# Performance work log

Measured on AMD Instinct MI355X. Metric: run time of the kernel, lower is better.

## Reference

```python
import jax, jax.numpy as jnp
import numpy as np

B, T, D = 32, 512, 768
K, H = 256, 512


def setup_inputs() -> dict:
    key = jax.random.key(0)
    ks = jax.random.split(key, 5)
    s = 0.02  # keep pre-activations in a sane range
    return {
        "inputs": jax.random.normal(ks[0], (B, T, D), jnp.float32),
        "W_x": jax.random.normal(ks[1], (K + 1, 4 * H), jnp.float32) * s,
        "W_h": jax.random.normal(ks[2], (H, 4 * H), jnp.float32) * s,
        "b_lstm": jnp.zeros((4 * H,), jnp.float32),
        "W_key": jax.random.normal(ks[3], (H, K), jnp.float32) * s,
        "b_key": jnp.zeros((K,), jnp.float32),
        "W_g": jax.random.normal(ks[4], (H, 1), jnp.float32) * s,
        "b_g": jnp.zeros((1,), jnp.float32),
        "conf_gain": jnp.ones((), jnp.float32),
        "conf_bias": jnp.zeros((), jnp.float32),
    }


def reference(inputs, W_x, W_h, b_lstm, W_key, b_key, W_g, b_g, conf_gain, conf_bias):
    Bq, Tq, Dq = inputs.shape
    Kq = W_key.shape[1]
    Hq = W_h.shape[0]
    t_idx = jnp.arange(Tq)
    xs = jnp.transpose(inputs, (1, 0, 2))  # [T, B, D]

    def step(carry, xt):
        t, x = xt  # t: scalar step index, x: [B, D]
        key_r, h, c, M_k, M_v = carry
        # Keras LSTMCell (gate order i, f, c, o); input is previous key_r [B, K+1]
        z = key_r @ W_x + h @ W_h + b_lstm
        i, f, g_c, o = jnp.split(z, 4, axis=-1)
        i = jax.nn.sigmoid(i)
        f = jax.nn.sigmoid(f)
        g_c = jnp.tanh(g_c)
        o = jax.nn.sigmoid(o)
        c = f * c + i * g_c
        h = o * jnp.tanh(c)  # lstm_out == hidden in Keras LSTMCell
        key_w = h @ W_key + b_key            # [B, K]
        g = jax.nn.sigmoid(h @ W_g + b_g)    # [B, 1]
        # similarity attention over all previously written memory slots
        sim = jnp.einsum('bd,tbd->bt', x, M_v)          # [B, T]
        mask = (t_idx < t)[None, :]                     # valid slots only
        w_k = jax.nn.softmax(jnp.where(mask, sim, -1e30), axis=1)
        c_k = jax.nn.sigmoid(sim * conf_gain + conf_bias)
        aug = jnp.concatenate([jnp.transpose(M_k, (1, 0, 2)), c_k[:, :, None]], axis=2)  # [B, T, K+1]
        key_r_new = jnp.where(t > 0, g * jnp.einsum('bt,btk->bk', w_k, aug), 0.0)
        M_k = M_k.at[t].set(key_w)
        M_v = M_v.at[t].set(x)
        return (key_r_new, h, c, M_k, M_v), None

    init = (
        jnp.zeros((Bq, Kq + 1), inputs.dtype),
        jnp.zeros((Bq, Hq), inputs.dtype),
        jnp.zeros((Bq, Hq), inputs.dtype),
        jnp.zeros((Tq, Bq, Kq), inputs.dtype),
        jnp.zeros((Tq, Bq, Dq), inputs.dtype),
    )
    (key_r, h, c, M_k, M_v), _ = jax.lax.scan(step, init, (t_idx, xs))
    return h  # final lstm_out
```

## Files before the change

kernel.cpp:

```cpp
#include <hip/hip_runtime.h>
#include <math.h>

#define BQ 32
#define TQ 512
#define DQ 768
#define KQ 256
#define HQ 512
#define G4 2048
#define SROW 772
#define NWG 512
#define NTHR 256
#define NBG 4

typedef float f32x4 __attribute__((ext_vector_type(4)));

__device__ __forceinline__ void waitcnt0() {
  asm volatile("s_waitcnt vmcnt(0) lgkmcnt(0)" ::: "memory");
}
__device__ __forceinline__ void st_agent(float* p, float v) {
  asm volatile("global_store_dword %0, %1, off sc0 sc1" :: "v"(p), "v"(v) : "memory");
}
__device__ __forceinline__ int ld_flag(const int* p) {
  int v;
  asm volatile("global_load_dword %0, %1, off sc0 sc1\ns_waitcnt vmcnt(0)"
               : "=v"(v) : "v"(p) : "memory");
  return v;
}
__device__ __forceinline__ void wg_wait(const int* flags, int target) {
  const int lane = threadIdx.x & 63;
  for (;;) {
    int v = ld_flag(flags + lane);
    if (__all(v >= target)) break;
    __builtin_amdgcn_s_sleep(1);
  }
  __syncthreads();
}
__device__ __forceinline__ void wg_signal(int* flag, int val) {
  waitcnt0();
  __syncthreads();
  if (threadIdx.x == 0)
    asm volatile("global_store_dword %0, %1, off sc0 sc1" :: "v"(flag), "v"(val) : "memory");
}
__device__ __forceinline__ float sigm(float x) { return 1.f / (1.f + __expf(-x)); }

__global__ void __launch_bounds__(256) gram_k(const float* __restrict__ X,
                                              float* __restrict__ Gm) {
  __shared__ __align__(16) float As[64 * 33];
  __shared__ __align__(16) float Bs[64 * 33];
  const int bid = blockIdx.x;
  const int b = blockIdx.y;
  int I = 0, base = 0;
  while (base + I + 1 <= bid) { base += I + 1; ++I; }
  const int J = bid - base;
  const int t0 = I * 64, u0 = J * 64;
  const float* Xb = X + (size_t)b * TQ * DQ;
  const int ty = threadIdx.x >> 4, tx = threadIdx.x & 15;
  const int sc = threadIdx.x & 31, sr = threadIdx.x >> 5;
  float acc[4][4];
#pragma unroll
  for (int i = 0; i < 4; ++i)
#pragma unroll
    for (int j = 0; j < 4; ++j) acc[i][j] = 0.f;
  for (int k0 = 0; k0 < DQ; k0 += 32) {
#pragma unroll
    for (int rr = 0; rr < 8; ++rr) {
      const int r = rr * 8 + sr;
      As[r * 33 + sc] = Xb[(size_t)(t0 + r) * DQ + k0 + sc];
      Bs[r * 33 + sc] = Xb[(size_t)(u0 + r) * DQ + k0 + sc];
    }
    __syncthreads();
#pragma unroll
    for (int k = 0; k < 32; ++k) {
      float av[4], bv[4];
#pragma unroll
      for (int i = 0; i < 4; ++i) av[i] = As[(ty * 4 + i) * 33 + k];
#pragma unroll
      for (int j = 0; j < 4; ++j) bv[j] = Bs[(tx * 4 + j) * 33 + k];
#pragma unroll
      for (int i = 0; i < 4; ++i)
#pragma unroll
        for (int j = 0; j < 4; ++j) acc[i][j] += av[i] * bv[j];
    }
    __syncthreads();
  }
  float* gb = Gm + (size_t)b * TQ * TQ;
#pragma unroll
  for (int i = 0; i < 4; ++i) {
    f32x4 o;
    o.x = acc[i][0]; o.y = acc[i][1]; o.z = acc[i][2]; o.w = acc[i][3];
    *(f32x4*)&gb[(size_t)(t0 + ty * 4 + i) * TQ + u0 + tx * 4] = o;
  }
}

__global__ void __launch_bounds__(256) smax_k(float* __restrict__ Gm,
                                              float* __restrict__ Sv,
                                              const float* __restrict__ cgp,
                                              const float* __restrict__ cbp) {
  const int t = blockIdx.x + 1;
  const int b = blockIdx.y;
  const int tid = threadIdx.x;
  const int lane = tid & 63;
  const int wv = tid >> 6;
  __shared__ float row[TQ];
  __shared__ float r1[4], r2[4], r3[4];
  float* R = Gm + ((size_t)b * TQ + t) * TQ;
  const float cg = cgp[0], cb = cbp[0];
  for (int i = tid; i < t; i += 256) row[i] = R[i];
  __syncthreads();
  float m = -3e38f;
  for (int i = tid; i < t; i += 256) m = fmaxf(m, row[i]);
#pragma unroll
  for (int k = 1; k < 64; k <<= 1) m = fmaxf(m, __shfl_xor(m, k));
  if (lane == 0) r1[wv] = m;
  __syncthreads();
  m = fmaxf(fmaxf(r1[0], r1[1]), fmaxf(r1[2], r1[3]));
  float s = 0.f, sck = 0.f;
  for (int i = tid; i < t; i += 256) {
    const float r = row[i];
    const float e = __expf(r - m);
    const float ck = 1.f / (1.f + __expf(-(r * cg + cb)));
    row[i] = e; s += e; sck += e * ck;
  }
#pragma unroll
  for (int k = 1; k < 64; k <<= 1) { s += __shfl_xor(s, k); sck += __shfl_xor(sck, k); }
  if (lane == 0) { r2[wv] = s; r3[wv] = sck; }
  __syncthreads();
  s = r2[0] + r2[1] + r2[2] + r2[3];
  sck = r3[0] + r3[1] + r3[2] + r3[3];
  const float inv = 1.f / s;
  for (int i = tid; i < t; i += 256) R[i] = row[i] * inv;
  if (tid == 0) Sv[(size_t)b * TQ + t] = sck * inv;
}

__global__ void __launch_bounds__(NTHR, 2) esbn_scan(
    const float* __restrict__ Wx, const float* __restrict__ Wh,
    const float* __restrict__ bl, const float* __restrict__ Wk,
    const float* __restrict__ bk, const float* __restrict__ Wg,
    const float* __restrict__ bgp, const float* __restrict__ Wmat,
    const float* __restrict__ Sv, float* buf, int* flagsX, int* flagsY,
    float* __restrict__ out) {
  __shared__ __align__(16) float st[NBG * SROW];
  __shared__ __align__(16) float wrow[NBG * TQ];
  __shared__ __align__(16) float Mk_s[16 * 520];
  __shared__ __align__(16) float wkey_s[4 * 520];
  __shared__ float wgv[HQ];
  __shared__ __align__(16) float zred[4 * 8 * 4 * 4];
  __shared__ float c_s[NBG * 8];
  __shared__ float gg_s[NBG];
  __shared__ float A_s[NBG * 4];
  __shared__ float bl_s[32];
  __shared__ float bk_s[4];
  __shared__ float bg_s;

  const int tid = threadIdx.x;
  const int wg = blockIdx.x & 63;
  const int grp = blockIdx.x >> 6;
  const int b0 = grp * NBG;
  const int dc = tid >> 3;
  const int cg = tid & 7;

  int colg[4];
#pragma unroll
  for (int j = 0; j < 4; ++j) {
    const int c = cg * 4 + j;
    colg[j] = (c >> 3) * HQ + wg * 8 + (c & 7);
  }
  f32x4 wh[16], wxr[8], wxl;
#pragma unroll
  for (int i = 0; i < 16; ++i) {
    const int d = (i << 5) + dc;
    wh[i].x = Wh[(size_t)d * G4 + colg[0]];
    wh[i].y = Wh[(size_t)d * G4 + colg[1]];
    wh[i].z = Wh[(size_t)d * G4 + colg[2]];
    wh[i].w = Wh[(size_t)d * G4 + colg[3]];
  }
#pragma unroll
  for (int i = 0; i < 8; ++i) {
    const int d = (i << 5) + dc;
    wxr[i].x = Wx[(size_t)d * G4 + colg[0]];
    wxr[i].y = Wx[(size_t)d * G4 + colg[1]];
    wxr[i].z = Wx[(size_t)d * G4 + colg[2]];
    wxr[i].w = Wx[(size_t)d * G4 + colg[3]];
  }
  wxl.x = wxl.y = wxl.z = wxl.w = 0.f;
  if (dc == 0) {
    wxl.x = Wx[(size_t)256 * G4 + colg[0]];
    wxl.y = Wx[(size_t)256 * G4 + colg[1]];
    wxl.z = Wx[(size_t)256 * G4 + colg[2]];
    wxl.w = Wx[(size_t)256 * G4 + colg[3]];
  }
  for (int i = tid; i < NBG * SROW; i += NTHR) st[i] = 0.f;
  for (int i = tid; i < 16 * 520; i += NTHR) Mk_s[i] = 0.f;
  for (int i = tid; i < 4 * 520; i += NTHR) {
    const int kl = i / 520, u = i - kl * 520;
    wkey_s[i] = (u < HQ) ? Wk[(size_t)u * KQ + wg * 4 + kl] : 0.f;
  }
  for (int i = tid; i < HQ; i += NTHR) wgv[i] = Wg[i];
  if (tid < 32) bl_s[tid] = bl[(tid >> 3) * HQ + wg * 8 + (tid & 7)];
  if (tid < 4) bk_s[tid] = bk[wg * 4 + tid];
  if (tid == 0) bg_s = bgp[0];
  if (tid < NBG * 8) c_s[tid] = 0.f;
  if (tid < NBG * 4) A_s[tid] = 0.f;
  __syncthreads();

  int* fx = flagsX + grp * 64;
  int* fy = flagsY + grp * 64;
  const int yb = tid >> 6;
  const int ykl = (tid >> 4) & 3;
  const int ytc = tid & 15;
  const int lt = tid & 63;

  for (int t = 0; t < TQ; ++t) {
    const int p = t & 1, pn = p ^ 1;
    f32x4 acc[NBG];
#pragma unroll
    for (int b = 0; b < NBG; ++b) { acc[b].x = 0.f; acc[b].y = 0.f; acc[b].z = 0.f; acc[b].w = 0.f; }
#pragma unroll
    for (int i = 0; i < 16; ++i) {
      const f32x4 w = wh[i];
      const int d = (i << 5) + dc;
#pragma unroll
      for (int b = 0; b < NBG; ++b) acc[b] += st[b * SROW + d] * w;
    }
    wg_wait(fy, t);
    {
      float* base = buf + (size_t)(p * BQ + b0) * SROW;
      const int r0 = tid / 65, o0 = tid - r0 * 65;
      const float* q0 = base + r0 * SROW + 512 + (o0 << 2);
      f32x4 u0, u1;
      u1.x = u1.y = u1.z = u1.w = 0.f;
      asm volatile("global_load_dwordx4 %0, %1, off sc0 sc1" : "=v"(u0) : "v"(q0));
      if (tid < 4) {
        const int j1 = tid + 256;
        const int r1 = j1 / 65, o1 = j1 - r1 * 65;
        const float* q1 = base + r1 * SROW + 512 + (o1 << 2);
        asm volatile("global_load_dwordx4 %0, %1, off sc0 sc1" : "=v"(u1) : "v"(q1));
      }
      asm volatile("s_waitcnt vmcnt(0)" : "+v"(u0), "+v"(u1) : : "memory");
      *(f32x4*)&st[r0 * SROW + 512 + (o0 << 2)] = u0;
      if (tid < 4) {
        const int j1 = tid + 256;
        const int r1 = j1 / 65, o1 = j1 - r1 * 65;
        *(f32x4*)&st[r1 * SROW + 512 + (o1 << 2)] = u1;
      }
    }
    __syncthreads();
#pragma unroll
    for (int i = 0; i < 8; ++i) {
      const f32x4 w = wxr[i];
      const int d = 512 + (i << 5) + dc;
#pragma unroll
      for (int b = 0; b < NBG; ++b) acc[b] += st[b * SROW + d] * w;
    }
    if (dc == 0) {
#pragma unroll
      for (int b = 0; b < NBG; ++b) acc[b] += st[b * SROW + 768] * wxl;
    }
#pragma unroll
    for (int m = 8; m <= 32; m <<= 1) {
#pragma unroll
      for (int b = 0; b < NBG; ++b) {
        acc[b].x += __shfl_xor(acc[b].x, m);
        acc[b].y += __shfl_xor(acc[b].y, m);
        acc[b].z += __shfl_xor(acc[b].z, m);
        acc[b].w += __shfl_xor(acc[b].w, m);
      }
    }
    if (lt < 8) {
      const int wv = tid >> 6;
#pragma unroll
      for (int b = 0; b < NBG; ++b)
        *(f32x4*)&zred[((wv * 8 + lt) * 4 + b) * 4] = acc[b];
    }
    __syncthreads();
    if (tid < 32) {
      const int b = tid >> 3, u = tid & 7;
      float zg[4];
#pragma unroll
      for (int g = 0; g < 4; ++g) {
        const int cgi = g * 2 + (u >> 2), comp = u & 3;
        float z = bl_s[g * 8 + u];
#pragma unroll
        for (int wv = 0; wv < 4; ++wv) z += zred[((wv * 8 + cgi) * 4 + b) * 4 + comp];
        zg[g] = z;
      }
      const float gi = sigm(zg[0]);
      const float gf = sigm(zg[1]);
      const float go = sigm(zg[3]);
      const float cn = gf * c_s[tid] + gi * tanhf(zg[2]);
      const float hv = go * tanhf(cn);
      c_s[tid] = cn;
      st_agent(buf + (size_t)(pn * BQ + b0 + b) * SROW + wg * 8 + u, hv);
      if (t == TQ - 1) out[(size_t)(b0 + b) * HQ + wg * 8 + u] = hv;
    }
    wg_signal(&fx[wg], t + 1);
    if (t == TQ - 1) break;

    if (t > 0) {
      const float* wr = Wmat + ((size_t)(b0 + yb) * TQ + t) * TQ;
#pragma unroll
      for (int k = 0; k < 8; ++k) {
        const int u = lt + (k << 6);
        wrow[yb * TQ + u] = (u < t) ? wr[u] : 0.f;
      }
    }
    __syncthreads();
    float accA = 0.f;
    if (t > 0) {
      const float* mk = &Mk_s[(yb * 4 + ykl) * 520];
      const float* wb = &wrow[yb * TQ];
#pragma unroll
      for (int j = 0; j < 32; ++j) {
        const int u = ytc + (j << 4);
        accA += wb[u] * mk[u];
      }
      accA += __shfl_xor(accA, 1);
      accA += __shfl_xor(accA, 2);
      accA += __shfl_xor(accA, 4);
      accA += __shfl_xor(accA, 8);
    }
    if (ytc == 0) A_s[yb * 4 + ykl] = accA;
    wg_wait(fx, t + 1);
    {
      float* base = buf + (size_t)(pn * BQ + b0) * SROW;
      f32x4 v0, v1;
      const int i0 = tid, i1 = tid + 256;
      const float* p0 = base + (i0 >> 7) * SROW + ((i0 & 127) << 2);
      const float* p1v = base + (i1 >> 7) * SROW + ((i1 & 127) << 2);
      asm volatile("global_load_dwordx4 %0, %1, off sc0 sc1" : "=v"(v0) : "v"(p0));
      asm volatile("global_load_dwordx4 %0, %1, off sc0 sc1" : "=v"(v1) : "v"(p1v));
      asm volatile("s_waitcnt vmcnt(0)" : "+v"(v0), "+v"(v1) : : "memory");
      *(f32x4*)&st[(i0 >> 7) * SROW + ((i0 & 127) << 2)] = v0;
      *(f32x4*)&st[(i1 >> 7) * SROW + ((i1 & 127) << 2)] = v1;
    }
    __syncthreads();
    {
      float a = 0.f;
#pragma unroll
      for (int k = 0; k < 8; ++k) {
        const int u = lt + (k << 6);
        a += st[yb * SROW + u] * wgv[u];
      }
#pragma unroll
      for (int m = 1; m <= 32; m <<= 1) a += __shfl_xor(a, m);
      if (lt == 0) gg_s[yb] = sigm(a + bg_s);
    }
    __syncthreads();
    if (ytc == 0)
      st_agent(buf + (size_t)(pn * BQ + b0 + yb) * SROW + 512 + wg * 4 + ykl,
               gg_s[yb] * A_s[yb * 4 + ykl]);
    if (wg == 63 && lt == 0)
      st_agent(buf + (size_t)(pn * BQ + b0 + yb) * SROW + 512 + 256,
               gg_s[yb] * Sv[(size_t)(b0 + yb) * TQ + t]);
    wg_signal(&fy[wg], t + 1);
    {
      float kw = 0.f;
      const float* hrow = &st[yb * SROW];
      const float* wkr = &wkey_s[ykl * 520];
#pragma unroll
      for (int j = 0; j < 32; ++j) {
        const int u = ytc + (j << 4);
        kw += hrow[u] * wkr[u];
      }
      kw += __shfl_xor(kw, 1);
      kw += __shfl_xor(kw, 2);
      kw += __shfl_xor(kw, 4);
      kw += __shfl_xor(kw, 8);
      if (ytc == 0) Mk_s[(yb * 4 + ykl) * 520 + t] = kw + bk_s[ykl];
    }
  }
}

extern "C" void kernel_launch(void* const* d_in, const int* in_sizes, int n_in,
                              void* d_out, int out_size, void* d_ws, size_t ws_size,
                              hipStream_t stream) {
  (void)in_sizes; (void)n_in; (void)out_size; (void)ws_size;
  const float* X  = (const float*)d_in[0];
  const float* Wx = (const float*)d_in[1];
  const float* Wh = (const float*)d_in[2];
  const float* bl = (const float*)d_in[3];
  const float* Wk = (const float*)d_in[4];
  const float* bk = (const float*)d_in[5];
  const float* Wg = (const float*)d_in[6];
  const float* bg = (const float*)d_in[7];
  const float* cg = (const float*)d_in[8];
  const float* cb = (const float*)d_in[9];
  float* out = (float*)d_out;
  float* ws = (float*)d_ws;

  float* Gm = ws;
  float* Sv = ws + (size_t)8388608;
  float* buf = ws + (size_t)8404992;
  int* flagsX = (int*)(ws + (size_t)8454400);
  int* flagsY = flagsX + 512;

  hipMemsetAsync(Sv, 0, (size_t)(16384 + 49408 + 1024) * 4, stream);
  gram_k<<<dim3(36, BQ), dim3(256), 0, stream>>>(X, Gm);
  smax_k<<<dim3(TQ - 1, BQ), dim3(256), 0, stream>>>(Gm, Sv, cg, cb);

  void* args[] = {(void*)&Wx, (void*)&Wh, (void*)&bl, (void*)&Wk, (void*)&bk,
                  (void*)&Wg, (void*)&bg, (void*)&Gm, (void*)&Sv,
                  (void*)&buf, (void*)&flagsX, (void*)&flagsY, (void*)&out};
  hipError_t e = hipLaunchCooperativeKernel((const void*)esbn_scan, dim3(NWG),
                                            dim3(NTHR), args, 0, stream);
  if (e != hipSuccess) {
    esbn_scan<<<dim3(NWG), dim3(NTHR), 0, stream>>>(Wx, Wh, bl, Wk, bk, Wg, bg,
                                                    Gm, Sv, buf, flagsX,
                                                    flagsY, out);
  }
}
```

Before: 4.876 ms.

## Fold W_key into W_x and cut scan to one grid barrier per step

Precomputes Wc = W_key·W_x[:K] and bk·W_x so that key_r·W_x is rewritten as g·(attention-weighted h history)·Wc plus bias and confidence terms. Each workgroup stores its own h history slice in shared memory as int16 and computes the weighted history sum locally. This removes the second cross-workgroup flag wait and the per-step key projection. It also remaps blocks so a group's workgroups interleave. The risks are precision loss from 16-bit quantized h and an extra GEMM setup kernel.

```diff
diff --git a/kernel.cpp b/kernel.cpp
--- a/kernel.cpp
+++ b/kernel.cpp
@@ -7,10 +7,10 @@
 #define KQ 256
 #define HQ 512
 #define G4 2048
-#define SROW 772
 #define NWG 512
 #define NTHR 256
 #define NBG 4
+#define PROW 1028
 
 typedef float f32x4 __attribute__((ext_vector_type(4)));
 
@@ -24,6 +24,11 @@
   int v;
   asm volatile("global_load_dword %0, %1, off sc0 sc1\ns_waitcnt vmcnt(0)"
                : "=v"(v) : "v"(p) : "memory");
+  return v;
+}
+__device__ __forceinline__ f32x4 ldx4(const float* p) {
+  f32x4 v;
+  asm volatile("global_load_dwordx4 %0, %1, off sc0 sc1" : "=v"(v) : "v"(p) : "memory");
   return v;
 }
 __device__ __forceinline__ void wg_wait(const int* flags, int target) {
@@ -34,12 +39,6 @@
     __builtin_amdgcn_s_sleep(1);
   }
   __syncthreads();
-}
-__device__ __forceinline__ void wg_signal(int* flag, int val) {
-  waitcnt0();
-  __syncthreads();
-  if (threadIdx.x == 0)
-    asm volatile("global_store_dword %0, %1, off sc0 sc1" :: "v"(flag), "v"(val) : "memory");
 }
 __device__ __forceinline__ float sigm(float x) { return 1.f / (1.f + __expf(-x)); }
 
@@ -132,29 +131,79 @@
   if (tid == 0) Sv[(size_t)b * TQ + t] = sck * inv;
 }
 
+__global__ void __launch_bounds__(256) wcomb_k(const float* __restrict__ Wkey,
+                                               const float* __restrict__ Wx,
+                                               float* __restrict__ Wc) {
+  __shared__ __align__(16) float As[64 * 33];
+  __shared__ __align__(16) float Bs[64 * 33];
+  const int c0 = blockIdx.x * 64, u0 = blockIdx.y * 64;
+  const int ty = threadIdx.x >> 4, tx = threadIdx.x & 15;
+  const int sc = threadIdx.x & 31, sr = threadIdx.x >> 5;
+  float acc[4][4];
+#pragma unroll
+  for (int i = 0; i < 4; ++i)
+#pragma unroll
+    for (int j = 0; j < 4; ++j) acc[i][j] = 0.f;
+  for (int k0 = 0; k0 < KQ; k0 += 32) {
+#pragma unroll
+    for (int rr = 0; rr < 8; ++rr) {
+      const int r = rr * 8 + sr;
+      As[r * 33 + sc] = Wkey[(size_t)(u0 + r) * KQ + k0 + sc];
+      Bs[r * 33 + sc] = Wx[(size_t)(k0 + sc) * G4 + c0 + r];
+    }
+    __syncthreads();
+#pragma unroll
+    for (int k = 0; k < 32; ++k) {
+      float av[4], bv[4];
+#pragma unroll
+      for (int i = 0; i < 4; ++i) av[i] = As[(ty * 4 + i) * 33 + k];
+#pragma unroll
+      for (int j = 0; j < 4; ++j) bv[j] = Bs[(tx * 4 + j) * 33 + k];
+#pragma unroll
+      for (int i = 0; i < 4; ++i)
+#pragma unroll
+        for (int j = 0; j < 4; ++j) acc[i][j] += av[i] * bv[j];
+    }
+    __syncthreads();
+  }
+#pragma unroll
+  for (int i = 0; i < 4; ++i) {
+    f32x4 o;
+    o.x = acc[i][0]; o.y = acc[i][1]; o.z = acc[i][2]; o.w = acc[i][3];
+    *(f32x4*)&Wc[(size_t)(u0 + ty * 4 + i) * G4 + c0 + tx * 4] = o;
+  }
+}
+
+__global__ void __launch_bounds__(256) bkwx_k(const float* __restrict__ bk,
+                                              const float* __restrict__ Wx,
+                                              float* __restrict__ bw) {
+  const int col = blockIdx.x * 256 + threadIdx.x;
+  float a = 0.f;
+  for (int k = 0; k < KQ; ++k) a += bk[k] * Wx[(size_t)k * G4 + col];
+  bw[col] = a;
+}
+
 __global__ void __launch_bounds__(NTHR, 2) esbn_scan(
     const float* __restrict__ Wx, const float* __restrict__ Wh,
     const float* __restrict__ bl, const float* __restrict__ Wk,
     const float* __restrict__ bk, const float* __restrict__ Wg,
     const float* __restrict__ bgp, const float* __restrict__ Wmat,
-    const float* __restrict__ Sv, float* buf, int* flagsX, int* flagsY,
+    const float* __restrict__ Sv, const float* __restrict__ Wc,
+    const float* __restrict__ bw, float* buf, int* flags,
     float* __restrict__ out) {
-  __shared__ __align__(16) float st[NBG * SROW];
-  __shared__ __align__(16) float wrow[NBG * TQ];
-  __shared__ __align__(16) float Mk_s[16 * 520];
-  __shared__ __align__(16) float wkey_s[4 * 520];
+  __shared__ short hh[32 * 520];
+  __shared__ __align__(16) float st_h[NBG * 512];
+  __shared__ __align__(16) float st_q[NBG * 512];
+  __shared__ __align__(16) float wrow[NBG * 512];
   __shared__ float wgv[HQ];
-  __shared__ __align__(16) float zred[4 * 8 * 4 * 4];
-  __shared__ float c_s[NBG * 8];
-  __shared__ float gg_s[NBG];
-  __shared__ float A_s[NBG * 4];
-  __shared__ float bl_s[32];
-  __shared__ float bk_s[4];
+  __shared__ __align__(16) float zred[4 * 8 * 4 * 8];
+  __shared__ float bl_s[32], e_s[32], l_s[32], c_s[32];
+  __shared__ float gg_s[NBG], sv_s[NBG];
   __shared__ float bg_s;
 
   const int tid = threadIdx.x;
-  const int wg = blockIdx.x & 63;
-  const int grp = blockIdx.x >> 6;
+  const int grp = blockIdx.x & 7;
+  const int wg = blockIdx.x >> 3;
   const int b0 = grp * NBG;
   const int dc = tid >> 3;
   const int cg = tid & 7;
@@ -165,7 +214,7 @@
     const int c = cg * 4 + j;
     colg[j] = (c >> 3) * HQ + wg * 8 + (c & 7);
   }
-  f32x4 wh[16], wxr[8], wxl;
+  f32x4 wh[16], wc[16];
 #pragma unroll
   for (int i = 0; i < 16; ++i) {
     const int d = (i << 5) + dc;
@@ -174,199 +223,202 @@
     wh[i].z = Wh[(size_t)d * G4 + colg[2]];
     wh[i].w = Wh[(size_t)d * G4 + colg[3]];
   }
-#pragma unroll
-  for (int i = 0; i < 8; ++i) {
-    const int d = (i << 5) + dc;
-    wxr[i].x = Wx[(size_t)d * G4 + colg[0]];
-    wxr[i].y = Wx[(size_t)d * G4 + colg[1]];
-    wxr[i].z = Wx[(size_t)d * G4 + colg[2]];
-    wxr[i].w = Wx[(size_t)d * G4 + colg[3]];
-  }
-  wxl.x = wxl.y = wxl.z = wxl.w = 0.f;
-  if (dc == 0) {
-    wxl.x = Wx[(size_t)256 * G4 + colg[0]];
-    wxl.y = Wx[(size_t)256 * G4 + colg[1]];
-    wxl.z = Wx[(size_t)256 * G4 + colg[2]];
-    wxl.w = Wx[(size_t)256 * G4 + colg[3]];
-  }
-  for (int i = tid; i < NBG * SROW; i += NTHR) st[i] = 0.f;
-  for (int i = tid; i < 16 * 520; i += NTHR) Mk_s[i] = 0.f;
-  for (int i = tid; i < 4 * 520; i += NTHR) {
-    const int kl = i / 520, u = i - kl * 520;
-    wkey_s[i] = (u < HQ) ? Wk[(size_t)u * KQ + wg * 4 + kl] : 0.f;
-  }
+  if (Wc != nullptr) {
+#pragma unroll
+    for (int i = 0; i < 16; ++i) {
+      const int u = (i << 5) + dc;
+      wc[i].x = Wc[(size_t)u * G4 + colg[0]];
+      wc[i].y = Wc[(size_t)u * G4 + colg[1]];
+      wc[i].z = Wc[(size_t)u * G4 + colg[2]];
+      wc[i].w = Wc[(size_t)u * G4 + colg[3]];
+    }
+    if (tid < 32) {
+      const int gc = (tid >> 3) * HQ + wg * 8 + (tid & 7);
+      e_s[tid] = bw[gc];
+    }
+  } else {
+#pragma unroll
+    for (int i = 0; i < 16; ++i) { wc[i].x = wc[i].y = wc[i].z = wc[i].w = 0.f; }
+    f32x4 e4; e4.x = e4.y = e4.z = e4.w = 0.f;
+    for (int k = 0; k < KQ; ++k) {
+      f32x4 wxk;
+      wxk.x = Wx[(size_t)k * G4 + colg[0]];
+      wxk.y = Wx[(size_t)k * G4 + colg[1]];
+      wxk.z = Wx[(size_t)k * G4 + colg[2]];
+      wxk.w = Wx[(size_t)k * G4 + colg[3]];
+      e4 += bk[k] * wxk;
+#pragma unroll
+      for (int i = 0; i < 16; ++i) wc[i] += Wk[(size_t)((i << 5) + dc) * KQ + k] * wxk;
+    }
+    if (dc == 0) {
+      e_s[cg * 4 + 0] = e4.x; e_s[cg * 4 + 1] = e4.y;
+      e_s[cg * 4 + 2] = e4.z; e_s[cg * 4 + 3] = e4.w;
+    }
+  }
+  if (tid < 32) {
+    const int gc = (tid >> 3) * HQ + wg * 8 + (tid & 7);
+    bl_s[tid] = bl[gc];
+    l_s[tid] = Wx[(size_t)256 * G4 + gc];
+    c_s[tid] = 0.f;
+  }
+  for (int i = tid; i < 32 * 520; i += NTHR) hh[i] = 0;
   for (int i = tid; i < HQ; i += NTHR) wgv[i] = Wg[i];
-  if (tid < 32) bl_s[tid] = bl[(tid >> 3) * HQ + wg * 8 + (tid & 7)];
-  if (tid < 4) bk_s[tid] = bk[wg * 4 + tid];
   if (tid == 0) bg_s = bgp[0];
-  if (tid < NBG * 8) c_s[tid] = 0.f;
-  if (tid < NBG * 4) A_s[tid] = 0.f;
   __syncthreads();
 
-  int* fx = flagsX + grp * 64;
-  int* fy = flagsY + grp * 64;
+  int* fx = flags + grp * 64;
   const int yb = tid >> 6;
-  const int ykl = (tid >> 4) & 3;
-  const int ytc = tid & 15;
-  const int lt = tid & 63;
-
-  for (int t = 0; t < TQ; ++t) {
-    const int p = t & 1, pn = p ^ 1;
-    f32x4 acc[NBG];
-#pragma unroll
-    for (int b = 0; b < NBG; ++b) { acc[b].x = 0.f; acc[b].y = 0.f; acc[b].z = 0.f; acc[b].w = 0.f; }
+  const int yu = (tid >> 3) & 7;
+  const int ytc = tid & 7;
+  const float invS = 1.f / 32767.f;
+
+  for (int s = 0; s < TQ; ++s) {
+    const int p = s & 1, pn = p ^ 1;
+    {
+#pragma unroll
+      for (int k = 0; k < 2; ++k) {
+        const int f = k * 256 + tid;
+        const int b = f >> 7, off = (f & 127) << 2;
+        const float* src = Wmat + ((size_t)(b0 + b) * TQ + s) * TQ + off;
+        f32x4 v = *(const f32x4*)src;
+        v.x = (off + 0 < s) ? v.x : 0.f;
+        v.y = (off + 1 < s) ? v.y : 0.f;
+        v.z = (off + 2 < s) ? v.z : 0.f;
+        v.w = (off + 3 < s) ? v.w : 0.f;
+        *(f32x4*)&wrow[b * 512 + off] = v;
+      }
+      if (tid < 4) sv_s[tid] = (s >= 1) ? Sv[(size_t)(b0 + tid) * TQ + (s - 1)] : 0.f;
+    }
+    __syncthreads();
+    float pre = 0.f;
+    if (s > 0 && s < TQ - 1) {
+      const short2* hp = (const short2*)&hh[(yb * 8 + yu) * 520];
+      const float2* wp = (const float2*)&wrow[yb * 512];
+#pragma unroll
+      for (int j = 0; j < 32; ++j) {
+        const short2 hv2 = hp[ytc + 8 * j];
+        const float2 w2 = wp[ytc + 8 * j];
+        pre += w2.x * (float)hv2.x + w2.y * (float)hv2.y;
+      }
+      pre += __shfl_xor(pre, 1);
+      pre += __shfl_xor(pre, 2);
+      pre += __shfl_xor(pre, 4);
+      pre *= invS;
+    }
+    wg_wait(fx, s);
+    {
+      const float* base = buf + (size_t)(p * BQ + b0) * PROW;
+      const int off = tid << 2;
+      f32x4 v[4];
+#pragma unroll
+      for (int k = 0; k < 4; ++k) v[k] = ldx4(base + (size_t)k * PROW + off);
+      asm volatile("s_waitcnt vmcnt(0)"
+                   : "+v"(v[0]), "+v"(v[1]), "+v"(v[2]), "+v"(v[3]) :: "memory");
+#pragma unroll
+      for (int k = 0; k < 4; ++k) {
+        if (tid < 128) *(f32x4*)&st_h[k * 512 + off] = v[k];
+        else *(f32x4*)&st_q[k * 512 + off - 512] = v[k];
+      }
+    }
+    __syncthreads();
+    if (ytc == 0) {
+      const float hprev = st_h[yb * 512 + wg * 8 + yu];
+      if (s > 0) {
+        hh[(yb * 8 + yu) * 520 + (s - 1)] = (short)__float2int_rn(hprev * 32767.f);
+        if (s < TQ - 1) {
+          const float hb = pre + wrow[yb * 512 + (s - 1)] * hprev;
+          st_agent(buf + (size_t)(pn * BQ + b0 + yb) * PROW + 512 + wg * 8 + yu, hb);
+        }
+      } else if (s < TQ - 1) {
+        st_agent(buf + (size_t)(pn * BQ + b0 + yb) * PROW + 512 + wg * 8 + yu, 0.f);
+      }
+    }
+    {
+      float a = 0.f;
+      const int lt = tid & 63;
+#pragma unroll
+      for (int k = 0; k < 8; ++k) {
+        const int u = lt + (k << 6);
+        a += st_h[yb * 512 + u] * wgv[u];
+      }
+#pragma unroll
+      for (int m = 1; m <= 32; m <<= 1) a += __shfl_xor(a, m);
+      if (lt == 0) gg_s[yb] = sigm(a + bg_s);
+    }
+    f32x4 aH[NBG], aQ[NBG];
+#pragma unroll
+    for (int b = 0; b < NBG; ++b) {
+      aH[b].x = aH[b].y = aH[b].z = aH[b].w = 0.f;
+      aQ[b].x = aQ[b].y = aQ[b].z = aQ[b].w = 0.f;
+    }
 #pragma unroll
     for (int i = 0; i < 16; ++i) {
-      const f32x4 w = wh[i];
       const int d = (i << 5) + dc;
-#pragma unroll
-      for (int b = 0; b < NBG; ++b) acc[b] += st[b * SROW + d] * w;
-    }
-    wg_wait(fy, t);
+      const f32x4 w1 = wh[i], w2 = wc[i];
+#pragma unroll
+      for (int b = 0; b < NBG; ++b) {
+        aH[b] += st_h[b * 512 + d] * w1;
+        aQ[b] += st_q[b * 512 + d] * w2;
+      }
+    }
+#pragma unroll
+    for (int m = 8; m <= 32; m <<= 1) {
+#pragma unroll
+      for (int b = 0; b < NBG; ++b) {
+        aH[b].x += __shfl_xor(aH[b].x, m); aH[b].y += __shfl_xor(aH[b].y, m);
+        aH[b].z += __shfl_xor(aH[b].z, m); aH[b].w += __shfl_xor(aH[b].w, m);
+        aQ[b].x += __shfl_xor(aQ[b].x, m); aQ[b].y += __shfl_xor(aQ[b].y, m);
+        aQ[b].z += __shfl_xor(aQ[b].z, m); aQ[b].w += __shfl_xor(aQ[b].w, m);
+      }
+    }
     {
-      float* base = buf + (size_t)(p * BQ + b0) * SROW;
-      const int r0 = tid / 65, o0 = tid - r0 * 65;
-      const float* q0 = base + r0 * SROW + 512 + (o0 << 2);
-      f32x4 u0, u1;
-      u1.x = u1.y = u1.z = u1.w = 0.f;
-      asm volatile("global_load_dwordx4 %0, %1, off sc0 sc1" : "=v"(u0) : "v"(q0));
-      if (tid < 4) {
-        const int j1 = tid + 256;
-        const int r1 = j1 / 65, o1 = j1 - r1 * 65;
-        const float* q1 = base + r1 * SROW + 512 + (o1 << 2);
-        asm volatile("global_load_dwordx4 %0, %1, off sc0 sc1" : "=v"(u1) : "v"(q1));
-      }
-      asm volatile("s_waitcnt vmcnt(0)" : "+v"(u0), "+v"(u1) : : "memory");
-      *(f32x4*)&st[r0 * SROW + 512 + (o0 << 2)] = u0;
-      if (tid < 4) {
-        const int j1 = tid + 256;
-        const int r1 = j1 / 65, o1 = j1 - r1 * 65;
-        *(f32x4*)&st[r1 * SROW + 512 + (o1 << 2)] = u1;
-      }
-    }
-    __syncthreads();
-#pragma unroll
-    for (int i = 0; i < 8; ++i) {
-      const f32x4 w = wxr[i];
-      const int d = 512 + (i << 5) + dc;
-#pragma unroll
-      for (int b = 0; b < NBG; ++b) acc[b] += st[b * SROW + d] * w;
-    }
-    if (dc == 0) {
-#pragma unroll
-      for (int b = 0; b < NBG; ++b) acc[b] += st[b * SROW + 768] * wxl;
-    }
-#pragma unroll
-    for (int m = 8; m <= 32; m <<= 1) {
-#pragma unroll
-      for (int b = 0; b < NBG; ++b) {
-        acc[b].x += __shfl_xor(acc[b].x, m);
-        acc[b].y += __shfl_xor(acc[b].y, m);
-        acc[b].z += __shfl_xor(acc[b].z, m);
-        acc[b].w += __shfl_xor(acc[b].w, m);
-      }
-    }
-    if (lt < 8) {
-      const int wv = tid >> 6;
-#pragma unroll
-      for (int b = 0; b < NBG; ++b)
-        *(f32x4*)&zred[((wv * 8 + lt) * 4 + b) * 4] = acc[b];
+      const int lt = tid & 63;
+      if (lt < 8) {
+        const int wv = tid >> 6;
+#pragma unroll
+        for (int b = 0; b < NBG; ++b) {
+          *(f32x4*)&zred[((wv * 8 + lt) * 4 + b) * 8] = aH[b];
+          *(f32x4*)&zred[((wv * 8 + lt) * 4 + b) * 8 + 4] = aQ[b];
+        }
+      }
     }
     __syncthreads();
     if (tid < 32) {
       const int b = tid >> 3, u = tid & 7;
+      const float g = (s > 0) ? gg_s[b] : 0.f;
+      const float es = (s >= 2) ? 1.f : 0.f;
+      const float sv = sv_s[b];
       float zg[4];
 #pragma unroll
-      for (int g = 0; g < 4; ++g) {
-        const int cgi = g * 2 + (u >> 2), comp = u & 3;
-        float z = bl_s[g * 8 + u];
-#pragma unroll
-        for (int wv = 0; wv < 4; ++wv) z += zred[((wv * 8 + cgi) * 4 + b) * 4 + comp];
-        zg[g] = z;
-      }
-      const float gi = sigm(zg[0]);
+      for (int gi = 0; gi < 4; ++gi) {
+        const int c = gi * 8 + u, cgi = c >> 2, comp = c & 3;
+        float sH = 0.f, sQ = 0.f;
+#pragma unroll
+        for (int wv = 0; wv < 4; ++wv) {
+          sH += zred[((wv * 8 + cgi) * 4 + b) * 8 + comp];
+          sQ += zred[((wv * 8 + cgi) * 4 + b) * 8 + 4 + comp];
+        }
+        zg[gi] = sH + g * (sQ + es * e_s[c] + sv * l_s[c]) + bl_s[c];
+      }
+      const float gi_ = sigm(zg[0]);
       const float gf = sigm(zg[1]);
       const float go = sigm(zg[3]);
-      const float cn = gf * c_s[tid] + gi * tanhf(zg[2]);
+      const float cn = gf * c_s[tid] + gi_ * tanhf(zg[2]);
       const float hv = go * tanhf(cn);
       c_s[tid] = cn;
-      st_agent(buf + (size_t)(pn * BQ + b0 + b) * SROW + wg * 8 + u, hv);
-      if (t == TQ - 1) out[(size_t)(b0 + b) * HQ + wg * 8 + u] = hv;
-    }
-    wg_signal(&fx[wg], t + 1);
-    if (t == TQ - 1) break;
-
-    if (t > 0) {
-      const float* wr = Wmat + ((size_t)(b0 + yb) * TQ + t) * TQ;
-#pragma unroll
-      for (int k = 0; k < 8; ++k) {
-        const int u = lt + (k << 6);
-        wrow[yb * TQ + u] = (u < t) ? wr[u] : 0.f;
-      }
-    }
-    __syncthreads();
-    float accA = 0.f;
-    if (t > 0) {
-      const float* mk = &Mk_s[(yb * 4 + ykl) * 520];
-      const float* wb = &wrow[yb * TQ];
-#pragma unroll
-      for (int j = 0; j < 32; ++j) {
-        const int u = ytc + (j << 4);
-        accA += wb[u] * mk[u];
-      }
-      accA += __shfl_xor(accA, 1);
-      accA += __shfl_xor(accA, 2);
-      accA += __shfl_xor(accA, 4);
-      accA += __shfl_xor(accA, 8);
-    }
-    if (ytc == 0) A_s[yb * 4 + ykl] = accA;
-    wg_wait(fx, t + 1);
-    {
-      float* base = buf + (size_t)(pn * BQ + b0) * SROW;
-      f32x4 v0, v1;
-      const int i0 = tid, i1 = tid + 256;
-      const float* p0 = base + (i0 >> 7) * SROW + ((i0 & 127) << 2);
-      const float* p1v = base + (i1 >> 7) * SROW + ((i1 & 127) << 2);
-      asm volatile("global_load_dwordx4 %0, %1, off sc0 sc1" : "=v"(v0) : "v"(p0));
-      asm volatile("global_load_dwordx4 %0, %1, off sc0 sc1" : "=v"(v1) : "v"(p1v));
-      asm volatile("s_waitcnt vmcnt(0)" : "+v"(v0), "+v"(v1) : : "memory");
-      *(f32x4*)&st[(i0 >> 7) * SROW + ((i0 & 127) << 2)] = v0;
-      *(f32x4*)&st[(i1 >> 7) * SROW + ((i1 & 127) << 2)] = v1;
-    }
-    __syncthreads();
-    {
-      float a = 0.f;
-#pragma unroll
-      for (int k = 0; k < 8; ++k) {
-        const int u = lt + (k << 6);
-        a += st[yb * SROW + u] * wgv[u];
-      }
-#pragma unroll
-      for (int m = 1; m <= 32; m <<= 1) a += __shfl_xor(a, m);
-      if (lt == 0) gg_s[yb] = sigm(a + bg_s);
-    }
-    __syncthreads();
-    if (ytc == 0)
-      st_agent(buf + (size_t)(pn * BQ + b0 + yb) * SROW + 512 + wg * 4 + ykl,
-               gg_s[yb] * A_s[yb * 4 + ykl]);
-    if (wg == 63 && lt == 0)
-      st_agent(buf + (size_t)(pn * BQ + b0 + yb) * SROW + 512 + 256,
-               gg_s[yb] * Sv[(size_t)(b0 + yb) * TQ + t]);
-    wg_signal(&fy[wg], t + 1);
-    {
-      float kw = 0.f;
-      const float* hrow = &st[yb * SROW];
-      const float* wkr = &wkey_s[ykl * 520];
-#pragma unroll
-      for (int j = 0; j < 32; ++j) {
-        const int u = ytc + (j << 4);
-        kw += hrow[u] * wkr[u];
-      }
-      kw += __shfl_xor(kw, 1);
-      kw += __shfl_xor(kw, 2);
-      kw += __shfl_xor(kw, 4);
-      kw += __shfl_xor(kw, 8);
-      if (ytc == 0) Mk_s[(yb * 4 + ykl) * 520 + t] = kw + bk_s[ykl];
+      if (s == TQ - 1) {
+        out[(size_t)(b0 + b) * HQ + wg * 8 + u] = hv;
+      } else {
+        st_agent(buf + (size_t)(pn * BQ + b0 + b) * PROW + wg * 8 + u, hv);
+      }
+    }
+    if (s == TQ - 1) break;
+    waitcnt0();
+    __syncthreads();
+    if (tid == 0) {
+      int* fp = &fx[wg];
+      const int val = s + 1;
+      asm volatile("global_store_dword %0, %1, off sc0 sc1" :: "v"(fp), "v"(val) : "memory");
     }
   }
 }
@@ -374,7 +426,7 @@
 extern "C" void kernel_launch(void* const* d_in, const int* in_sizes, int n_in,
                               void* d_out, int out_size, void* d_ws, size_t ws_size,
                               hipStream_t stream) {
-  (void)in_sizes; (void)n_in; (void)out_size; (void)ws_size;
+  (void)in_sizes; (void)n_in; (void)out_size;
   const float* X  = (const float*)d_in[0];
   const float* Wx = (const float*)d_in[1];
   const float* Wh = (const float*)d_in[2];
@@ -388,24 +440,33 @@
   float* out = (float*)d_out;
   float* ws = (float*)d_ws;
 
+  size_t off = 8388608;
   float* Gm = ws;
-  float* Sv = ws + (size_t)8388608;
-  float* buf = ws + (size_t)8404992;
-  int* flagsX = (int*)(ws + (size_t)8454400);
-  int* flagsY = flagsX + 512;
-
-  hipMemsetAsync(Sv, 0, (size_t)(16384 + 49408 + 1024) * 4, stream);
+  float* Wc = nullptr;
+  float* bw = nullptr;
+  const size_t need_wc = (size_t)(8388608 + 1048576 + 2048 + 16384 + 65792 + 512) * 4;
+  const bool havewc = ws_size >= need_wc;
+  if (havewc) { Wc = ws + off; off += 1048576; bw = ws + off; off += 2048; }
+  float* Sv = ws + off; off += 16384;
+  float* buf = ws + off; off += 65792;
+  int* flags = (int*)(ws + off);
+
+  hipMemsetAsync(Sv, 0, (size_t)(16384 + 65792 + 512) * 4, stream);
   gram_k<<<dim3(36, BQ), dim3(256), 0, stream>>>(X, Gm);
   smax_k<<<dim3(TQ - 1, BQ), dim3(256), 0, stream>>>(Gm, Sv, cg, cb);
+  if (havewc) {
+    wcomb_k<<<dim3(32, 8), dim3(256), 0, stream>>>(Wk, Wx, Wc);
+    bkwx_k<<<dim3(8), dim3(256), 0, stream>>>(bk, Wx, bw);
+  }
 
   void* args[] = {(void*)&Wx, (void*)&Wh, (void*)&bl, (void*)&Wk, (void*)&bk,
-                  (void*)&Wg, (void*)&bg, (void*)&Gm, (void*)&Sv,
-                  (void*)&buf, (void*)&flagsX, (void*)&flagsY, (void*)&out};
+                  (void*)&Wg, (void*)&bg, (void*)&Gm, (void*)&Sv, (void*)&Wc,
+                  (void*)&bw, (void*)&buf, (void*)&flags, (void*)&out};
   hipError_t e = hipLaunchCooperativeKernel((const void*)esbn_scan, dim3(NWG),
                                             dim3(NTHR), args, 0, stream);
   if (e != hipSuccess) {
     esbn_scan<<<dim3(NWG), dim3(NTHR), 0, stream>>>(Wx, Wh, bl, Wk, bk, Wg, bg,
-                                                    Gm, Sv, buf, flagsX,
-                                                    flagsY, out);
-  }
-}
+                                                    Gm, Sv, Wc, bw, buf, flags,
+                                                    out);
+  }
+}
```

New measurement: 6.363 ms. +30.5%, slower.
